# Performance work log

Hardware: AMD Instinct MI355X
Metric: run time of the kernel (lower is better)

The kernel has to match this reference:

```python
import jax, jax.numpy as jnp
import numpy as np

B, F, V, E, H, L, D = 1024, 4096, 20000, 512, 1024, 20, 4


def _lstm_step(x, h, c, Wih, Whh, bih, bhh):
    # torch nn.LSTMCell gate order: i, f, g, o
    gates = x @ Wih.T + bih + h @ Whh.T + bhh
    i, f, g, o = jnp.split(gates, 4, axis=-1)
    c = jax.nn.sigmoid(f) * c + jax.nn.sigmoid(i) * jnp.tanh(g)
    h = jax.nn.sigmoid(o) * jnp.tanh(c)
    return h, c


def setup_inputs() -> dict:
    key = jax.random.key(0)
    ks = jax.random.split(key, 12)
    s = 0.02  # small init so exp(scores) stays sane
    return {
        "target": jax.random.normal(ks[0], (B, F), jnp.float32),
        "distractors": jax.random.normal(ks[1], (D, B, F), jnp.float32),
        "start_token_idx": 1,
        "max_sentence_length": L,
        # Sender params
        "emb_s": jax.random.normal(ks[2], (V, E), jnp.float32) * s,
        "Wih_s": jax.random.normal(ks[3], (4 * H, E), jnp.float32) * s,
        "Whh_s": jax.random.normal(ks[4], (4 * H, H), jnp.float32) * s,
        "bih_s": jnp.zeros((4 * H,), jnp.float32),
        "bhh_s": jnp.zeros((4 * H,), jnp.float32),
        "aff_s_W": jax.random.normal(ks[5], (H, F), jnp.float32) * s,
        "aff_s_b": jnp.zeros((H,), jnp.float32),
        "probs_W": jax.random.normal(ks[6], (V, H), jnp.float32) * s,
        "probs_b": jnp.zeros((V,), jnp.float32),
        # Receiver params
        "emb_r": jax.random.normal(ks[7], (V, E), jnp.float32) * s,
        "Wih_r": jax.random.normal(ks[8], (4 * H, E), jnp.float32) * s,
        "Whh_r": jax.random.normal(ks[9], (4 * H, H), jnp.float32) * s,
        "bih_r": jnp.zeros((4 * H,), jnp.float32),
        "bhh_r": jnp.zeros((4 * H,), jnp.float32),
        "aff_r_W": jax.random.normal(ks[10], (F, H), jnp.float32) * s,
        "aff_r_b": jnp.zeros((F,), jnp.float32),
    }


def reference(target, distractors, start_token_idx, max_sentence_length,
              emb_s, Wih_s, Whh_s, bih_s, bhh_s, aff_s_W, aff_s_b, probs_W, probs_b,
              emb_r, Wih_r, Whh_r, bih_r, bhh_r, aff_r_W, aff_r_b):
    b = target.shape[0]
    # ---- Sender (greedy / eval path): per-step LSTMCell as lax.scan ----
    h0 = target @ aff_s_W.T + aff_s_b              # [B, H]
    c0 = jnp.zeros_like(h0)
    w0 = jnp.broadcast_to(emb_s[start_token_idx], (b, emb_s.shape[1]))

    def s_step(carry, _):
        h, c, w = carry
        h, c = _lstm_step(w, h, c, Wih_s, Whh_s, bih_s, bhh_s)
        logits = h @ probs_W.T + probs_b            # [B, V]
        logp = jax.nn.log_softmax(logits, axis=-1)
        w_idx = jnp.argmax(logits, axis=-1)         # greedy token
        lp = jnp.take_along_axis(logp, w_idx[:, None], axis=1)[:, 0]
        return (h, c, emb_s[w_idx]), (w_idx, lp)

    _, (message, lps) = jax.lax.scan(s_step, (h0, c0, w0), None, length=max_sentence_length)
    log_prob = lps[-1]                              # log_prob of last sampled token, [B]

    # ---- Receiver: consume message tokens with second LSTMCell scan ----
    def r_step(carry, w_idx):
        h, c = carry
        h, c = _lstm_step(emb_r[w_idx], h, c, Wih_r, Whh_r, bih_r, bhh_r)
        return (h, c), None

    (hr, _), _ = jax.lax.scan(r_step, (jnp.zeros_like(h0), jnp.zeros_like(h0)), message)
    r = hr @ aff_r_W.T + aff_r_b                    # [B, F]

    # ---- Hinge loss over distractors ----
    r_t = r.T                                       # [F, B]
    ts = target @ r_t                               # [B, B]
    ds = jnp.einsum('dbf,fk->dbk', distractors, r_t)  # [D, B, B]
    hinge = jnp.maximum(0.0, 1.0 - ts[None] + ds).sum(0)  # [B, B]
    loss = jnp.mean(jnp.mean(-hinge * log_prob[None, :], axis=1))

    target_prob = jnp.mean(jnp.exp(ts), axis=1)     # [B]
    dist_prob = jnp.mean(jnp.exp(ds), axis=2)       # [D, B]
    all_probs = jnp.concatenate([target_prob[:, None], dist_prob.T], axis=1)  # [B, 1+D]
    accuracy = jnp.mean((jnp.argmax(all_probs, axis=1) == 0).astype(jnp.float32))
    return loss, accuracy
```

## Files before the change

kernel.cpp:

```cpp
#include <hip/hip_runtime.h>
#include <cmath>

#define B_ 1024
#define F_ 4096
#define V_ 20000
#define E_ 512
#define H_ 1024
#define L_ 20
#define D_ 4

typedef __bf16 bf16x8 __attribute__((ext_vector_type(8)));
typedef float  f32x4  __attribute__((ext_vector_type(4)));

#define BM 128
#define BN 128
#define BK 32

#define VPAD 20096

__device__ __forceinline__ void remap_block(int& bm, int& bn)
{
    const int nbx  = gridDim.x;
    const int nby  = gridDim.y;
    const int nwg  = nbx * nby;
    const int flat = blockIdx.y * nbx + blockIdx.x;
    const int q = nwg >> 3, r = nwg & 7;
    const int xcd = flat & 7, lead = flat >> 3;
    const int wgid = (xcd < r ? xcd * (q + 1) : r * (q + 1) + (xcd - r) * q) + lead;
    bm = (wgid % nby) * BM;
    bn = (wgid / nby) * BN;
}

__device__ __forceinline__ void gld_lds16(const void* g, void* l)
{
    __builtin_amdgcn_global_load_lds(
        (const __attribute__((address_space(1))) void*)g,
        (__attribute__((address_space(3))) void*)l, 16, 0, 0);
}

__global__ __launch_bounds__(256, 2) void gemm_nt_split(
    const float* __restrict__ A1, const float* __restrict__ W1, int K1,
    const float* __restrict__ A2, const float* __restrict__ W2, int K2,
    const float* __restrict__ b1, const float* __restrict__ b2,
    float* __restrict__ C, int M, int N)
{
    __shared__ __align__(16) __bf16 As_hi[BM][BK];
    __shared__ __align__(16) __bf16 As_lo[BM][BK];
    __shared__ __align__(16) __bf16 Ws_hi[BN][BK];
    __shared__ __align__(16) __bf16 Ws_lo[BN][BK];

    const int tid  = threadIdx.x;
    int bm, bn;
    remap_block(bm, bn);
    const int srow = tid >> 1;
    const int scol = (tid & 1) * 16;
    const int lane = tid & 63;
    const int wv   = tid >> 6;
    const int wm   = (wv & 1) * 64;
    const int wn   = (wv >> 1) * 64;
    const int fm   = lane & 15;
    const int fq   = lane >> 4;

    const bool wok = (bn + srow) < N;

    f32x4 acc[4][4];
#pragma unroll
    for (int i = 0; i < 4; ++i)
#pragma unroll
        for (int j = 0; j < 4; ++j) acc[i][j] = (f32x4){0.f, 0.f, 0.f, 0.f};

#pragma unroll 1
    for (int s = 0; s < 2; ++s) {
        const float* A = s ? A2 : A1;
        const float* W = s ? W2 : W1;
        const int    K = s ? K2 : K1;
        if (!A) continue;
        const float* Arow = A + (size_t)(bm + srow) * K;
        const float* Wrow = W + (size_t)(bn + srow) * K;

        for (int k0 = 0; k0 < K; k0 += BK) {
            float av[16], wvv[16];
            const float* ap = Arow + k0 + scol;
            *(float4*)&av[0]   = *(const float4*)(ap + 0);
            *(float4*)&av[4]   = *(const float4*)(ap + 4);
            *(float4*)&av[8]   = *(const float4*)(ap + 8);
            *(float4*)&av[12]  = *(const float4*)(ap + 12);
            if (wok) {
                const float* wp = Wrow + k0 + scol;
                *(float4*)&wvv[0]  = *(const float4*)(wp + 0);
                *(float4*)&wvv[4]  = *(const float4*)(wp + 4);
                *(float4*)&wvv[8]  = *(const float4*)(wp + 8);
                *(float4*)&wvv[12] = *(const float4*)(wp + 12);
            } else {
#pragma unroll
                for (int v = 0; v < 16; ++v) wvv[v] = 0.f;
            }
            __syncthreads();

#pragma unroll
            for (int u = 0; u < 16; u += 8) {
                bf16x8 hh, ll;
#pragma unroll
                for (int v = 0; v < 8; ++v) {
                    float x = av[u + v];
                    __bf16 h = (__bf16)x;
                    hh[v] = h;
                    ll[v] = (__bf16)(x - (float)h);
                }
                *(bf16x8*)&As_hi[srow][scol + u] = hh;
                *(bf16x8*)&As_lo[srow][scol + u] = ll;
            }
#pragma unroll
            for (int u = 0; u < 16; u += 8) {
                bf16x8 hh, ll;
#pragma unroll
                for (int v = 0; v < 8; ++v) {
                    float x = wvv[u + v];
                    __bf16 h = (__bf16)x;
                    hh[v] = h;
                    ll[v] = (__bf16)(x - (float)h);
                }
                *(bf16x8*)&Ws_hi[srow][scol + u] = hh;
                *(bf16x8*)&Ws_lo[srow][scol + u] = ll;
            }
            __syncthreads();

            bf16x8 ah[4], al[4];
#pragma unroll
            for (int i = 0; i < 4; ++i) {
                ah[i] = *(const bf16x8*)&As_hi[wm + i * 16 + fm][fq * 8];
                al[i] = *(const bf16x8*)&As_lo[wm + i * 16 + fm][fq * 8];
            }
#pragma unroll
            for (int j = 0; j < 4; ++j) {
                bf16x8 bh = *(const bf16x8*)&Ws_hi[wn + j * 16 + fm][fq * 8];
                bf16x8 bl = *(const bf16x8*)&Ws_lo[wn + j * 16 + fm][fq * 8];
#pragma unroll
                for (int i = 0; i < 4; ++i) {
                    acc[i][j] = __builtin_amdgcn_mfma_f32_16x16x32_bf16(
                        al[i], bh, acc[i][j], 0, 0, 0);
                    acc[i][j] = __builtin_amdgcn_mfma_f32_16x16x32_bf16(
                        ah[i], bl, acc[i][j], 0, 0, 0);
                    acc[i][j] = __builtin_amdgcn_mfma_f32_16x16x32_bf16(
                        ah[i], bh, acc[i][j], 0, 0, 0);
                }
            }
        }
    }

#pragma unroll
    for (int j = 0; j < 4; ++j) {
        int col = bn + wn + j * 16 + fm;
        if (col >= N) continue;
        float badd = (b1 ? b1[col] : 0.f) + (b2 ? b2[col] : 0.f);
#pragma unroll
        for (int i = 0; i < 4; ++i) {
            int row0 = bm + wm + i * 16 + fq * 4;
            f32x4 v = acc[i][j];
#pragma unroll
            for (int r = 0; r < 4; ++r)
                C[(size_t)(row0 + r) * N + col] = v[r] + badd;
        }
    }
}

__global__ __launch_bounds__(256, 3) void gemm_nt_planes(
    const __bf16* __restrict__ Ah1, const __bf16* __restrict__ Al1,
    const __bf16* __restrict__ Wh1, const __bf16* __restrict__ Wl1, int K1,
    const __bf16* __restrict__ Ah2, const __bf16* __restrict__ Al2,
    const __bf16* __restrict__ Wh2, const __bf16* __restrict__ Wl2, int K2,
    const float* __restrict__ b1, const float* __restrict__ b2,
    float* __restrict__ C, int M, int N)
{
    __shared__ __align__(16) __bf16 As_hi[BM][BK];
    __shared__ __align__(16) __bf16 As_lo[BM][BK];
    __shared__ __align__(16) __bf16 Ws_hi[BN][BK];
    __shared__ __align__(16) __bf16 Ws_lo[BN][BK];

    const int tid  = threadIdx.x;
    int bm, bn;
    remap_block(bm, bn);
    const int srow = tid >> 2;
    const int scol = (tid & 3) * 8;
    const int lane = tid & 63;
    const int wv   = tid >> 6;
    const int wm   = (wv & 1) * 64;
    const int wn   = (wv >> 1) * 64;
    const int fm   = lane & 15;
    const int fq   = lane >> 4;

    f32x4 acc[4][4];
#pragma unroll
    for (int i = 0; i < 4; ++i)
#pragma unroll
        for (int j = 0; j < 4; ++j) acc[i][j] = (f32x4){0.f, 0.f, 0.f, 0.f};

#pragma unroll 1
    for (int s = 0; s < 2; ++s) {
        const __bf16* Ah = s ? Ah2 : Ah1;
        const __bf16* Al = s ? Al2 : Al1;
        const __bf16* Wh = s ? Wh2 : Wh1;
        const __bf16* Wl = s ? Wl2 : Wl1;
        const int     K  = s ? K2  : K1;
        if (!Ah) continue;
        const size_t aoff  = (size_t)(bm + srow) * K + scol;
        const size_t woff  = (size_t)(bn + srow) * K + scol;
        const size_t step  = (size_t)64 * K;

        for (int k0 = 0; k0 < K; k0 += BK) {
            __syncthreads();
            gld_lds16(Ah + aoff + k0,        &As_hi[srow][scol]);
            gld_lds16(Ah + aoff + k0 + step, &As_hi[srow + 64][scol]);
            gld_lds16(Al + aoff + k0,        &As_lo[srow][scol]);
            gld_lds16(Al + aoff + k0 + step, &As_lo[srow + 64][scol]);
            gld_lds16(Wh + woff + k0,        &Ws_hi[srow][scol]);
            gld_lds16(Wh + woff + k0 + step, &Ws_hi[srow + 64][scol]);
            gld_lds16(Wl + woff + k0,        &Ws_lo[srow][scol]);
            gld_lds16(Wl + woff + k0 + step, &Ws_lo[srow + 64][scol]);
            __syncthreads();

            bf16x8 ah[4], al[4];
#pragma unroll
            for (int i = 0; i < 4; ++i) {
                ah[i] = *(const bf16x8*)&As_hi[wm + i * 16 + fm][fq * 8];
                al[i] = *(const bf16x8*)&As_lo[wm + i * 16 + fm][fq * 8];
            }
#pragma unroll
            for (int j = 0; j < 4; ++j) {
                bf16x8 bh = *(const bf16x8*)&Ws_hi[wn + j * 16 + fm][fq * 8];
                bf16x8 bl = *(const bf16x8*)&Ws_lo[wn + j * 16 + fm][fq * 8];
#pragma unroll
                for (int i = 0; i < 4; ++i) {
                    acc[i][j] = __builtin_amdgcn_mfma_f32_16x16x32_bf16(
                        al[i], bh, acc[i][j], 0, 0, 0);
                    acc[i][j] = __builtin_amdgcn_mfma_f32_16x16x32_bf16(
                        ah[i], bl, acc[i][j], 0, 0, 0);
                    acc[i][j] = __builtin_amdgcn_mfma_f32_16x16x32_bf16(
                        ah[i], bh, acc[i][j], 0, 0, 0);
                }
            }
        }
    }

#pragma unroll
    for (int j = 0; j < 4; ++j) {
        int col = bn + wn + j * 16 + fm;
        if (col >= N) continue;
        float badd = (b1 ? b1[col] : 0.f) + (b2 ? b2[col] : 0.f);
#pragma unroll
        for (int i = 0; i < 4; ++i) {
            int row0 = bm + wm + i * 16 + fq * 4;
            f32x4 v = acc[i][j];
#pragma unroll
            for (int r = 0; r < 4; ++r)
                C[(size_t)(row0 + r) * N + col] = v[r] + badd;
        }
    }
}

__global__ __launch_bounds__(256) void split_planes(
    const float* __restrict__ src, __bf16* __restrict__ hi,
    __bf16* __restrict__ lo, long n8)
{
    long i = (long)blockIdx.x * 256 + threadIdx.x;
    if (i >= n8) return;
    float4 a = ((const float4*)src)[2 * i];
    float4 b = ((const float4*)src)[2 * i + 1];
    float v[8] = {a.x, a.y, a.z, a.w, b.x, b.y, b.z, b.w};
    bf16x8 hh, ll;
#pragma unroll
    for (int j = 0; j < 8; ++j) {
        float x = v[j];
        __bf16 h = (__bf16)x;
        hh[j] = h;
        ll[j] = (__bf16)(x - (float)h);
    }
    ((bf16x8*)hi)[i] = hh;
    ((bf16x8*)lo)[i] = ll;
}

__global__ __launch_bounds__(256) void lstm_pointwise(
    const float* __restrict__ gates, float* __restrict__ c, float* __restrict__ h,
    __bf16* __restrict__ hhi, __bf16* __restrict__ hlo)
{
    int i = blockIdx.x * blockDim.x + threadIdx.x;
    if (i >= B_ * H_) return;
    int b = i / H_, k = i % H_;
    const float* g = gates + (size_t)b * 4 * H_;
    float gi = g[k], gf = g[H_ + k], gg = g[2 * H_ + k], go = g[3 * H_ + k];
    float si = 1.f / (1.f + expf(-gi));
    float sf = 1.f / (1.f + expf(-gf));
    float so = 1.f / (1.f + expf(-go));
    float cn = sf * c[i] + si * tanhf(gg);
    c[i] = cn;
    float hv = so * tanhf(cn);
    h[i] = hv;
    if (hhi) {
        __bf16 hh = (__bf16)hv;
        hhi[i] = hh;
        hlo[i] = (__bf16)(hv - (float)hh);
    }
}

__global__ __launch_bounds__(256) void row_argmax_lse(
    const float* __restrict__ logits, int* __restrict__ tok,
    float* __restrict__ lp, int need_lp)
{
    int b = blockIdx.x;
    const float4* row4 = (const float4*)(logits + (size_t)b * V_);
    int tid = threadIdx.x;
    float m = -INFINITY; int mi = 0;
    float lm = -INFINITY, ls = 0.f;
    for (int j4 = tid; j4 < V_ / 4; j4 += 256) {
        float4 q = row4[j4];
        float vv[4] = {q.x, q.y, q.z, q.w};
#pragma unroll
        for (int u = 0; u < 4; ++u) {
            float v = vv[u];
            if (v > m) { m = v; mi = j4 * 4 + u; }
            if (need_lp) {
                if (v > lm) { ls = ls * expf(lm - v) + 1.f; lm = v; }
                else ls += expf(v - lm);
            }
        }
    }
    __shared__ float sm[256]; __shared__ int si[256];
    __shared__ float slm[256], sls[256];
    sm[tid] = m; si[tid] = mi; slm[tid] = lm; sls[tid] = ls;
    __syncthreads();
    for (int s = 128; s > 0; s >>= 1) {
        if (tid < s) {
            float vm = sm[tid + s]; int vi = si[tid + s];
            if (vm > sm[tid] || (vm == sm[tid] && vi < si[tid])) {
                sm[tid] = vm; si[tid] = vi;
            }
            if (need_lp) {
                float am = slm[tid], as = sls[tid];
                float bm2 = slm[tid + s], bs = sls[tid + s];
                if (am >= bm2) {
                    sls[tid] = as + bs * expf(bm2 - am);
                } else {
                    sls[tid] = bs + as * expf(am - bm2);
                    slm[tid] = bm2;
                }
            }
        }
        __syncthreads();
    }
    if (tid == 0) {
        tok[b] = si[0];
        if (need_lp) lp[b] = sm[0] - (slm[0] + logf(sls[0]));
    }
}

__global__ __launch_bounds__(128) void gather_emb(
    const float* __restrict__ emb, const int* __restrict__ tok,
    float* __restrict__ out)
{
    int b = blockIdx.x;
    int t = tok[b];
    const float4* src = (const float4*)(emb + (size_t)t * E_);
    float4* dst = (float4*)(out + (size_t)b * E_);
    for (int e = threadIdx.x; e < E_ / 4; e += blockDim.x) dst[e] = src[e];
}

__global__ __launch_bounds__(128) void broadcast_emb(
    const float* __restrict__ emb, const int* __restrict__ sidx,
    float* __restrict__ out)
{
    int b = blockIdx.x;
    int t = sidx[0];
    const float4* src = (const float4*)(emb + (size_t)t * E_);
    float4* dst = (float4*)(out + (size_t)b * E_);
    for (int e = threadIdx.x; e < E_ / 4; e += blockDim.x) dst[e] = src[e];
}

__device__ __forceinline__ void emb_row_split(
    const float* __restrict__ emb, int t, int b, int i,
    __bf16* __restrict__ whi, __bf16* __restrict__ wlo)
{
    const float4* src = (const float4*)(emb + (size_t)t * E_);
    float4 a = src[2 * i], c2 = src[2 * i + 1];
    float v[8] = {a.x, a.y, a.z, a.w, c2.x, c2.y, c2.z, c2.w};
    bf16x8 hh, ll;
#pragma unroll
    for (int j = 0; j < 8; ++j) {
        float x = v[j];
        __bf16 h = (__bf16)x;
        hh[j] = h;
        ll[j] = (__bf16)(x - (float)h);
    }
    ((bf16x8*)(whi + (size_t)b * E_))[i] = hh;
    ((bf16x8*)(wlo + (size_t)b * E_))[i] = ll;
}

__global__ __launch_bounds__(64) void gather_emb_planes(
    const float* __restrict__ emb, const int* __restrict__ tok,
    __bf16* __restrict__ whi, __bf16* __restrict__ wlo)
{
    emb_row_split(emb, tok[blockIdx.x], blockIdx.x, threadIdx.x, whi, wlo);
}

__global__ __launch_bounds__(64) void broadcast_emb_planes(
    const float* __restrict__ emb, const int* __restrict__ sidx,
    __bf16* __restrict__ whi, __bf16* __restrict__ wlo)
{
    emb_row_split(emb, sidx[0], blockIdx.x, threadIdx.x, whi, wlo);
}

__global__ __launch_bounds__(256) void zero_f32(float* __restrict__ p, int n)
{
    int i = blockIdx.x * blockDim.x + threadIdx.x;
    if (i < n) p[i] = 0.f;
}

__global__ __launch_bounds__(256) void loss_rows(
    const float* __restrict__ sc, const float* __restrict__ lp,
    float* __restrict__ loss_part, float* __restrict__ acc_flag)
{
    int i = blockIdx.x; int tid = threadIdx.x;
    const float* tsrow = sc + (size_t)i * B_;
    float lsum = 0.f, tps = 0.f;
    float dps[4] = {0.f, 0.f, 0.f, 0.f};
    for (int j = tid; j < B_; j += 256) {
        float tsv = tsrow[j];
        float hv = 0.f;
#pragma unroll
        for (int d = 0; d < 4; ++d) {
            float dv = sc[((size_t)(1 + d) * B_ + i) * B_ + j];
            float t = 1.f - tsv + dv;
            hv += (t > 0.f) ? t : 0.f;
            dps[d] += expf(dv);
        }
        lsum += hv * lp[j];
        tps += expf(tsv);
    }
    __shared__ float red[6][256];
    red[0][tid] = lsum; red[1][tid] = tps;
    red[2][tid] = dps[0]; red[3][tid] = dps[1];
    red[4][tid] = dps[2]; red[5][tid] = dps[3];
    __syncthreads();
    for (int s = 128; s > 0; s >>= 1) {
        if (tid < s) {
#pragma unroll
            for (int q = 0; q < 6; ++q) red[q][tid] += red[q][tid + s];
        }
        __syncthreads();
    }
    if (tid == 0) {
        loss_part[i] = -red[0][0];
        float tp = red[1][0];
        float mx = fmaxf(fmaxf(red[2][0], red[3][0]), fmaxf(red[4][0], red[5][0]));
        acc_flag[i] = (tp >= mx) ? 1.f : 0.f;
    }
}

__global__ __launch_bounds__(256) void finalize_k(
    const float* __restrict__ loss_part, const float* __restrict__ acc_flag,
    float* __restrict__ out)
{
    int tid = threadIdx.x;
    float ls = 0.f, ac = 0.f;
    for (int i = tid; i < B_; i += 256) { ls += loss_part[i]; ac += acc_flag[i]; }
    __shared__ float s1[256], s2[256];
    s1[tid] = ls; s2[tid] = ac;
    __syncthreads();
    for (int s = 128; s > 0; s >>= 1) {
        if (tid < s) { s1[tid] += s1[tid + s]; s2[tid] += s2[tid + s]; }
        __syncthreads();
    }
    if (tid == 0) {
        out[0] = s1[0] / ((float)B_ * (float)B_);
        out[1] = s2[0] / (float)B_;
    }
}

extern "C" void kernel_launch(void* const* d_in, const int* in_sizes, int n_in,
                              void* d_out, int out_size, void* d_ws, size_t ws_size,
                              hipStream_t stream)
{
    const float* target    = (const float*)d_in[0];
    const float* distract  = (const float*)d_in[1];
    const int*   start_tok = (const int*)d_in[2];
    const float* emb_s   = (const float*)d_in[4];
    const float* Wih_s   = (const float*)d_in[5];
    const float* Whh_s   = (const float*)d_in[6];
    const float* bih_s   = (const float*)d_in[7];
    const float* bhh_s   = (const float*)d_in[8];
    const float* aff_s_W = (const float*)d_in[9];
    const float* aff_s_b = (const float*)d_in[10];
    const float* probs_W = (const float*)d_in[11];
    const float* probs_b = (const float*)d_in[12];
    const float* emb_r   = (const float*)d_in[13];
    const float* Wih_r   = (const float*)d_in[14];
    const float* Whh_r   = (const float*)d_in[15];
    const float* bih_r   = (const float*)d_in[16];
    const float* bhh_r   = (const float*)d_in[17];
    const float* aff_r_W = (const float*)d_in[18];
    const float* aff_r_b = (const float*)d_in[19];

    float* ws = (float*)d_ws;
    const size_t OFF_HS     = 0;
    const size_t OFF_CS     = 1048576;
    const size_t OFF_WE     = 2097152;
    const size_t OFF_GATES  = 2621440;
    const size_t OFF_HR     = 6815744;
    const size_t OFF_CR     = 7864320;
    const size_t OFF_LP     = 8912896;
    const size_t OFF_LOSSP  = 8916992;
    const size_t OFF_ACCF   = 8921088;
    const size_t OFF_MSG    = 8925184;
    const size_t OFF_LOGITS = 9437184;
    const size_t OFF_R      = 9437184;
    const size_t OFF_SC     = 13631488;
    const size_t OFF_PROBS_HI = 29917184;
    const size_t OFF_PROBS_LO = 40206336;
    const size_t OFF_WIHS_HI  = 50495488;
    const size_t OFF_WIHS_LO  = 51544064;
    const size_t OFF_WHHS_HI  = 52592640;
    const size_t OFF_WHHS_LO  = 54689792;
    const size_t OFF_WIHR_HI  = 56786944;
    const size_t OFF_WIHR_LO  = 57835520;
    const size_t OFF_WHHR_HI  = 58884096;
    const size_t OFF_WHHR_LO  = 60981248;
    const size_t OFF_WEP_HI   = 63078400;
    const size_t OFF_WEP_LO   = 63340544;
    const size_t OFF_HSP_HI   = 63602688;
    const size_t OFF_HSP_LO   = 64126976;
    const size_t OFF_HRP_HI   = 64651264;
    const size_t OFF_HRP_LO   = 65175552;
    const size_t TOTAL_FLOATS = 65699840;

    float* h_s    = ws + OFF_HS;
    float* c_s    = ws + OFF_CS;
    float* w_e    = ws + OFF_WE;
    float* gates  = ws + OFF_GATES;
    float* h_r    = ws + OFF_HR;
    float* c_r    = ws + OFF_CR;
    float* lp     = ws + OFF_LP;
    float* lossp  = ws + OFF_LOSSP;
    float* accf   = ws + OFF_ACCF;
    int*   msg    = (int*)(ws + OFF_MSG);
    float* logits = ws + OFF_LOGITS;
    float* r_buf  = ws + OFF_R;
    float* sc     = ws + OFF_SC;

    auto gemm = [&](const float* A1, const float* W1, int K1,
                    const float* A2, const float* W2, int K2,
                    const float* b1, const float* b2,
                    float* C, int M, int N) {
        dim3 grid((N + BN - 1) / BN, M / BM);
        gemm_nt_split<<<grid, dim3(256), 0, stream>>>(A1, W1, K1, A2, W2, K2,
                                                      b1, b2, C, M, N);
    };

    const bool fast = ws_size >= TOTAL_FLOATS * sizeof(float);

    if (fast) {
        __bf16* probs_hi = (__bf16*)(ws + OFF_PROBS_HI);
        __bf16* probs_lo = (__bf16*)(ws + OFF_PROBS_LO);
        __bf16* wihs_hi  = (__bf16*)(ws + OFF_WIHS_HI);
        __bf16* wihs_lo  = (__bf16*)(ws + OFF_WIHS_LO);
        __bf16* whhs_hi  = (__bf16*)(ws + OFF_WHHS_HI);
        __bf16* whhs_lo  = (__bf16*)(ws + OFF_WHHS_LO);
        __bf16* wihr_hi  = (__bf16*)(ws + OFF_WIHR_HI);
        __bf16* wihr_lo  = (__bf16*)(ws + OFF_WIHR_LO);
        __bf16* whhr_hi  = (__bf16*)(ws + OFF_WHHR_HI);
        __bf16* whhr_lo  = (__bf16*)(ws + OFF_WHHR_LO);
        __bf16* we_hi    = (__bf16*)(ws + OFF_WEP_HI);
        __bf16* we_lo    = (__bf16*)(ws + OFF_WEP_LO);
        __bf16* hs_hi    = (__bf16*)(ws + OFF_HSP_HI);
        __bf16* hs_lo    = (__bf16*)(ws + OFF_HSP_LO);
        __bf16* hr_hi    = (__bf16*)(ws + OFF_HRP_HI);
        __bf16* hr_lo    = (__bf16*)(ws + OFF_HRP_LO);

        auto cvt = [&](const float* src, __bf16* hi, __bf16* lo, long n) {
            long n8 = n / 8;
            split_planes<<<(unsigned)((n8 + 255) / 256), 256, 0, stream>>>(
                src, hi, lo, n8);
        };
        auto gemmP = [&](const __bf16* Ah1, const __bf16* Al1,
                         const __bf16* Wh1, const __bf16* Wl1, int K1,
                         const __bf16* Ah2, const __bf16* Al2,
                         const __bf16* Wh2, const __bf16* Wl2, int K2,
                         const float* b1, const float* b2,
                         float* C, int M, int N) {
            dim3 grid((N + BN - 1) / BN, M / BM);
            gemm_nt_planes<<<grid, dim3(256), 0, stream>>>(
                Ah1, Al1, Wh1, Wl1, K1, Ah2, Al2, Wh2, Wl2, K2, b1, b2, C, M, N);
        };

        cvt(probs_W, probs_hi, probs_lo, (long)V_ * H_);
        cvt(Wih_s, wihs_hi, wihs_lo, (long)4 * H_ * E_);
        cvt(Whh_s, whhs_hi, whhs_lo, (long)4 * H_ * H_);
        cvt(Wih_r, wihr_hi, wihr_lo, (long)4 * H_ * E_);
        cvt(Whh_r, whhr_hi, whhr_lo, (long)4 * H_ * H_);
        {
            int padn = (VPAD - V_) * H_ / 2;
            zero_f32<<<(padn + 255) / 256, 256, 0, stream>>>(
                ws + OFF_PROBS_HI + (size_t)V_ * H_ / 2, padn);
            zero_f32<<<(padn + 255) / 256, 256, 0, stream>>>(
                ws + OFF_PROBS_LO + (size_t)V_ * H_ / 2, padn);
        }

        gemm(target, aff_s_W, F_, nullptr, nullptr, 0, aff_s_b, nullptr, h_s, B_, H_);
        cvt(h_s, hs_hi, hs_lo, (long)B_ * H_);
        zero_f32<<<(B_ * H_ + 255) / 256, 256, 0, stream>>>(c_s, B_ * H_);
        broadcast_emb_planes<<<B_, 64, 0, stream>>>(emb_s, start_tok, we_hi, we_lo);

        for (int t = 0; t < L_; ++t) {
            gemmP(we_hi, we_lo, wihs_hi, wihs_lo, E_,
                  hs_hi, hs_lo, whhs_hi, whhs_lo, H_,
                  bih_s, bhh_s, gates, B_, 4 * H_);
            lstm_pointwise<<<(B_ * H_ + 255) / 256, 256, 0, stream>>>(
                gates, c_s, h_s, hs_hi, hs_lo);
            gemmP(hs_hi, hs_lo, probs_hi, probs_lo, H_,
                  nullptr, nullptr, nullptr, nullptr, 0,
                  probs_b, nullptr, logits, B_, V_);
            row_argmax_lse<<<B_, 256, 0, stream>>>(logits, msg + (size_t)t * B_, lp,
                                                   (t == L_ - 1) ? 1 : 0);
            if (t < L_ - 1)
                gather_emb_planes<<<B_, 64, 0, stream>>>(emb_s, msg + (size_t)t * B_,
                                                         we_hi, we_lo);
        }

        zero_f32<<<(B_ * H_ + 255) / 256, 256, 0, stream>>>(h_r, B_ * H_);
        zero_f32<<<(B_ * H_ + 255) / 256, 256, 0, stream>>>(c_r, B_ * H_);
        zero_f32<<<(B_ * H_ / 2 + 255) / 256, 256, 0, stream>>>(
            ws + OFF_HRP_HI, B_ * H_ / 2);
        zero_f32<<<(B_ * H_ / 2 + 255) / 256, 256, 0, stream>>>(
            ws + OFF_HRP_LO, B_ * H_ / 2);
        for (int t = 0; t < L_; ++t) {
            gather_emb_planes<<<B_, 64, 0, stream>>>(emb_r, msg + (size_t)t * B_,
                                                     we_hi, we_lo);
            gemmP(we_hi, we_lo, wihr_hi, wihr_lo, E_,
                  hr_hi, hr_lo, whhr_hi, whhr_lo, H_,
                  bih_r, bhh_r, gates, B_, 4 * H_);
            lstm_pointwise<<<(B_ * H_ + 255) / 256, 256, 0, stream>>>(
                gates, c_r, h_r, hr_hi, hr_lo);
        }
    } else {
        gemm(target, aff_s_W, F_, nullptr, nullptr, 0, aff_s_b, nullptr, h_s, B_, H_);
        zero_f32<<<(B_ * H_ + 255) / 256, 256, 0, stream>>>(c_s, B_ * H_);
        broadcast_emb<<<B_, 128, 0, stream>>>(emb_s, start_tok, w_e);

        for (int t = 0; t < L_; ++t) {
            gemm(w_e, Wih_s, E_, h_s, Whh_s, H_, bih_s, bhh_s, gates, B_, 4 * H_);
            lstm_pointwise<<<(B_ * H_ + 255) / 256, 256, 0, stream>>>(
                gates, c_s, h_s, nullptr, nullptr);
            gemm(h_s, probs_W, H_, nullptr, nullptr, 0, probs_b, nullptr,
                 logits, B_, V_);
            row_argmax_lse<<<B_, 256, 0, stream>>>(logits, msg + (size_t)t * B_, lp,
                                                   (t == L_ - 1) ? 1 : 0);
            if (t < L_ - 1)
                gather_emb<<<B_, 128, 0, stream>>>(emb_s, msg + (size_t)t * B_, w_e);
        }

        zero_f32<<<(B_ * H_ + 255) / 256, 256, 0, stream>>>(h_r, B_ * H_);
        zero_f32<<<(B_ * H_ + 255) / 256, 256, 0, stream>>>(c_r, B_ * H_);
        for (int t = 0; t < L_; ++t) {
            gather_emb<<<B_, 128, 0, stream>>>(emb_r, msg + (size_t)t * B_, w_e);
            gemm(w_e, Wih_r, E_, h_r, Whh_r, H_, bih_r, bhh_r, gates, B_, 4 * H_);
            lstm_pointwise<<<(B_ * H_ + 255) / 256, 256, 0, stream>>>(
                gates, c_r, h_r, nullptr, nullptr);
        }
    }

    gemm(h_r, aff_r_W, H_, nullptr, nullptr, 0, aff_r_b, nullptr, r_buf, B_, F_);
    gemm(target, r_buf, F_, nullptr, nullptr, 0, nullptr, nullptr, sc, B_, B_);
    gemm(distract, r_buf, F_, nullptr, nullptr, 0, nullptr, nullptr,
         sc + (size_t)B_ * B_, D_ * B_, B_);

    loss_rows<<<B_, 256, 0, stream>>>(sc, lp, lossp, accf);
    finalize_k<<<1, 256, 0, stream>>>(lossp, accf, (float*)d_out);
}
```

Measured before the change: 6.718 ms.

## Use pre-split bf16 planes for tail GEMMs and 128x64 tiles for gate GEMMs

Templates the plane-based GEMM on tile shape and adds a 128x64 variant. The LSTM gate GEMMs (N=4096) switch to it to get more workgroups. When the workspace is large enough, the affine, receiver-output and score GEMMs are moved from the on-the-fly fp32 split kernel to precomputed hi/lo bf16 planes, and the target and distractor score GEMMs are merged into one launch. The split GEMM loses its XCD remap. The cost is extra conversion passes over target, distractors and the affine weights, plus a larger workspace requirement.

Result: faster. 6.216 ms (-7.5%).

```diff
diff --git a/kernel.cpp b/kernel.cpp
--- a/kernel.cpp
+++ b/kernel.cpp
@@ -18,19 +18,6 @@
 
 #define VPAD 20096
 
-__device__ __forceinline__ void remap_block(int& bm, int& bn)
-{
-    const int nbx  = gridDim.x;
-    const int nby  = gridDim.y;
-    const int nwg  = nbx * nby;
-    const int flat = blockIdx.y * nbx + blockIdx.x;
-    const int q = nwg >> 3, r = nwg & 7;
-    const int xcd = flat & 7, lead = flat >> 3;
-    const int wgid = (xcd < r ? xcd * (q + 1) : r * (q + 1) + (xcd - r) * q) + lead;
-    bm = (wgid % nby) * BM;
-    bn = (wgid / nby) * BN;
-}
-
 __device__ __forceinline__ void gld_lds16(const void* g, void* l)
 {
     __builtin_amdgcn_global_load_lds(
@@ -50,8 +37,8 @@
     __shared__ __align__(16) __bf16 Ws_lo[BN][BK];
 
     const int tid  = threadIdx.x;
-    int bm, bn;
-    remap_block(bm, bn);
+    const int bm   = blockIdx.y * BM;
+    const int bn   = blockIdx.x * BN;
     const int srow = tid >> 1;
     const int scol = (tid & 1) * 16;
     const int lane = tid & 63;
@@ -164,7 +151,8 @@
     }
 }
 
-__global__ __launch_bounds__(256, 3) void gemm_nt_planes(
+template<int TBM, int TBN>
+__global__ __launch_bounds__(256, 3) void gemm_nt_planes_t(
     const __bf16* __restrict__ Ah1, const __bf16* __restrict__ Al1,
     const __bf16* __restrict__ Wh1, const __bf16* __restrict__ Wl1, int K1,
     const __bf16* __restrict__ Ah2, const __bf16* __restrict__ Al2,
@@ -172,28 +160,39 @@
     const float* __restrict__ b1, const float* __restrict__ b2,
     float* __restrict__ C, int M, int N)
 {
-    __shared__ __align__(16) __bf16 As_hi[BM][BK];
-    __shared__ __align__(16) __bf16 As_lo[BM][BK];
-    __shared__ __align__(16) __bf16 Ws_hi[BN][BK];
-    __shared__ __align__(16) __bf16 Ws_lo[BN][BK];
+    constexpr int MI = TBM / 32;
+    constexpr int NJ = TBN / 32;
+
+    __shared__ __align__(16) __bf16 As_hi[TBM][BK];
+    __shared__ __align__(16) __bf16 As_lo[TBM][BK];
+    __shared__ __align__(16) __bf16 Ws_hi[TBN][BK];
+    __shared__ __align__(16) __bf16 Ws_lo[TBN][BK];
 
     const int tid  = threadIdx.x;
-    int bm, bn;
-    remap_block(bm, bn);
+    const int nbx  = gridDim.x;
+    const int nby  = gridDim.y;
+    const int nwg  = nbx * nby;
+    const int flat = blockIdx.y * nbx + blockIdx.x;
+    const int q = nwg >> 3, r = nwg & 7;
+    const int xcd = flat & 7, lead = flat >> 3;
+    const int wgid = (xcd < r ? xcd * (q + 1) : r * (q + 1) + (xcd - r) * q) + lead;
+    const int bm = (wgid % nby) * TBM;
+    const int bn = (wgid / nby) * TBN;
+
     const int srow = tid >> 2;
     const int scol = (tid & 3) * 8;
     const int lane = tid & 63;
     const int wv   = tid >> 6;
-    const int wm   = (wv & 1) * 64;
-    const int wn   = (wv >> 1) * 64;
+    const int wm   = (wv & 1) * (TBM / 2);
+    const int wn   = (wv >> 1) * (TBN / 2);
     const int fm   = lane & 15;
     const int fq   = lane >> 4;
 
-    f32x4 acc[4][4];
-#pragma unroll
-    for (int i = 0; i < 4; ++i)
-#pragma unroll
-        for (int j = 0; j < 4; ++j) acc[i][j] = (f32x4){0.f, 0.f, 0.f, 0.f};
+    f32x4 acc[MI][NJ];
+#pragma unroll
+    for (int i = 0; i < MI; ++i)
+#pragma unroll
+        for (int j = 0; j < NJ; ++j) acc[i][j] = (f32x4){0.f, 0.f, 0.f, 0.f};
 
 #pragma unroll 1
     for (int s = 0; s < 2; ++s) {
@@ -203,34 +202,35 @@
         const __bf16* Wl = s ? Wl2 : Wl1;
         const int     K  = s ? K2  : K1;
         if (!Ah) continue;
-        const size_t aoff  = (size_t)(bm + srow) * K + scol;
-        const size_t woff  = (size_t)(bn + srow) * K + scol;
-        const size_t step  = (size_t)64 * K;
+        const size_t aoff = (size_t)(bm + srow) * K + scol;
+        const size_t woff = (size_t)(bn + srow) * K + scol;
 
         for (int k0 = 0; k0 < K; k0 += BK) {
             __syncthreads();
-            gld_lds16(Ah + aoff + k0,        &As_hi[srow][scol]);
-            gld_lds16(Ah + aoff + k0 + step, &As_hi[srow + 64][scol]);
-            gld_lds16(Al + aoff + k0,        &As_lo[srow][scol]);
-            gld_lds16(Al + aoff + k0 + step, &As_lo[srow + 64][scol]);
-            gld_lds16(Wh + woff + k0,        &Ws_hi[srow][scol]);
-            gld_lds16(Wh + woff + k0 + step, &Ws_hi[srow + 64][scol]);
-            gld_lds16(Wl + woff + k0,        &Ws_lo[srow][scol]);
-            gld_lds16(Wl + woff + k0 + step, &Ws_lo[srow + 64][scol]);
+#pragma unroll
+            for (int u = 0; u < TBM; u += 64) {
+                gld_lds16(Ah + aoff + k0 + (size_t)u * K, &As_hi[srow + u][scol]);
+                gld_lds16(Al + aoff + k0 + (size_t)u * K, &As_lo[srow + u][scol]);
+            }
+#pragma unroll
+            for (int u = 0; u < TBN; u += 64) {
+                gld_lds16(Wh + woff + k0 + (size_t)u * K, &Ws_hi[srow + u][scol]);
+                gld_lds16(Wl + woff + k0 + (size_t)u * K, &Ws_lo[srow + u][scol]);
+            }
             __syncthreads();
 
-            bf16x8 ah[4], al[4];
-#pragma unroll
-            for (int i = 0; i < 4; ++i) {
+            bf16x8 ah[MI], al[MI];
+#pragma unroll
+            for (int i = 0; i < MI; ++i) {
                 ah[i] = *(const bf16x8*)&As_hi[wm + i * 16 + fm][fq * 8];
                 al[i] = *(const bf16x8*)&As_lo[wm + i * 16 + fm][fq * 8];
             }
 #pragma unroll
-            for (int j = 0; j < 4; ++j) {
+            for (int j = 0; j < NJ; ++j) {
                 bf16x8 bh = *(const bf16x8*)&Ws_hi[wn + j * 16 + fm][fq * 8];
                 bf16x8 bl = *(const bf16x8*)&Ws_lo[wn + j * 16 + fm][fq * 8];
 #pragma unroll
-                for (int i = 0; i < 4; ++i) {
+                for (int i = 0; i < MI; ++i) {
                     acc[i][j] = __builtin_amdgcn_mfma_f32_16x16x32_bf16(
                         al[i], bh, acc[i][j], 0, 0, 0);
                     acc[i][j] = __builtin_amdgcn_mfma_f32_16x16x32_bf16(
@@ -243,17 +243,17 @@
     }
 
 #pragma unroll
-    for (int j = 0; j < 4; ++j) {
+    for (int j = 0; j < NJ; ++j) {
         int col = bn + wn + j * 16 + fm;
         if (col >= N) continue;
         float badd = (b1 ? b1[col] : 0.f) + (b2 ? b2[col] : 0.f);
 #pragma unroll
-        for (int i = 0; i < 4; ++i) {
+        for (int i = 0; i < MI; ++i) {
             int row0 = bm + wm + i * 16 + fq * 4;
             f32x4 v = acc[i][j];
 #pragma unroll
-            for (int r = 0; r < 4; ++r)
-                C[(size_t)(row0 + r) * N + col] = v[r] + badd;
+            for (int rr = 0; rr < 4; ++rr)
+                C[(size_t)(row0 + rr) * N + col] = v[rr] + badd;
         }
     }
 }
@@ -530,6 +530,15 @@
     const size_t OFF_HRP_HI   = 64651264;
     const size_t OFF_HRP_LO   = 65175552;
     const size_t TOTAL_FLOATS = 65699840;
+    const size_t OFF_AFFS_HI = 65699840;
+    const size_t OFF_AFFS_LO = 67796992;
+    const size_t OFF_AFFR_HI = 69894144;
+    const size_t OFF_AFFR_LO = 71991296;
+    const size_t OFF_RP_HI   = 74088448;
+    const size_t OFF_RP_LO   = 76185600;
+    const size_t OFF_TD_HI   = 78282752;
+    const size_t OFF_TD_LO   = 88768512;
+    const size_t TOTAL2_FLOATS = 99254272;
 
     float* h_s    = ws + OFF_HS;
     float* c_s    = ws + OFF_CS;
@@ -554,7 +563,8 @@
                                                       b1, b2, C, M, N);
     };
 
-    const bool fast = ws_size >= TOTAL_FLOATS * sizeof(float);
+    const bool fast      = ws_size >= TOTAL_FLOATS * sizeof(float);
+    const bool fast_tail = ws_size >= TOTAL2_FLOATS * sizeof(float);
 
     if (fast) {
         __bf16* probs_hi = (__bf16*)(ws + OFF_PROBS_HI);
@@ -573,6 +583,14 @@
         __bf16* hs_lo    = (__bf16*)(ws + OFF_HSP_LO);
         __bf16* hr_hi    = (__bf16*)(ws + OFF_HRP_HI);
         __bf16* hr_lo    = (__bf16*)(ws + OFF_HRP_LO);
+        __bf16* affs_hi  = (__bf16*)(ws + OFF_AFFS_HI);
+        __bf16* affs_lo  = (__bf16*)(ws + OFF_AFFS_LO);
+        __bf16* affr_hi  = (__bf16*)(ws + OFF_AFFR_HI);
+        __bf16* affr_lo  = (__bf16*)(ws + OFF_AFFR_LO);
+        __bf16* rp_hi    = (__bf16*)(ws + OFF_RP_HI);
+        __bf16* rp_lo    = (__bf16*)(ws + OFF_RP_LO);
+        __bf16* td_hi    = (__bf16*)(ws + OFF_TD_HI);
+        __bf16* td_lo    = (__bf16*)(ws + OFF_TD_LO);
 
         auto cvt = [&](const float* src, __bf16* hi, __bf16* lo, long n) {
             long n8 = n / 8;
@@ -586,7 +604,17 @@
                          const float* b1, const float* b2,
                          float* C, int M, int N) {
             dim3 grid((N + BN - 1) / BN, M / BM);
-            gemm_nt_planes<<<grid, dim3(256), 0, stream>>>(
+            gemm_nt_planes_t<128, 128><<<grid, dim3(256), 0, stream>>>(
+                Ah1, Al1, Wh1, Wl1, K1, Ah2, Al2, Wh2, Wl2, K2, b1, b2, C, M, N);
+        };
+        auto gemmP64 = [&](const __bf16* Ah1, const __bf16* Al1,
+                           const __bf16* Wh1, const __bf16* Wl1, int K1,
+                           const __bf16* Ah2, const __bf16* Al2,
+                           const __bf16* Wh2, const __bf16* Wl2, int K2,
+                           const float* b1, const float* b2,
+                           float* C, int M, int N) {
+            dim3 grid((N + 63) / 64, M / BM);
+            gemm_nt_planes_t<128, 64><<<grid, dim3(256), 0, stream>>>(
                 Ah1, Al1, Wh1, Wl1, K1, Ah2, Al2, Wh2, Wl2, K2, b1, b2, C, M, N);
         };
 
@@ -602,16 +630,29 @@
             zero_f32<<<(padn + 255) / 256, 256, 0, stream>>>(
                 ws + OFF_PROBS_LO + (size_t)V_ * H_ / 2, padn);
         }
-
-        gemm(target, aff_s_W, F_, nullptr, nullptr, 0, aff_s_b, nullptr, h_s, B_, H_);
+        if (fast_tail) {
+            cvt(aff_s_W, affs_hi, affs_lo, (long)H_ * F_);
+            cvt(aff_r_W, affr_hi, affr_lo, (long)F_ * H_);
+            cvt(target, td_hi, td_lo, (long)B_ * F_);
+            cvt(distract, td_hi + (size_t)B_ * F_, td_lo + (size_t)B_ * F_,
+                (long)D_ * B_ * F_);
+        }
+
+        if (fast_tail)
+            gemmP64(td_hi, td_lo, affs_hi, affs_lo, F_,
+                    nullptr, nullptr, nullptr, nullptr, 0,
+                    aff_s_b, nullptr, h_s, B_, H_);
+        else
+            gemm(target, aff_s_W, F_, nullptr, nullptr, 0, aff_s_b, nullptr,
+                 h_s, B_, H_);
         cvt(h_s, hs_hi, hs_lo, (long)B_ * H_);
         zero_f32<<<(B_ * H_ + 255) / 256, 256, 0, stream>>>(c_s, B_ * H_);
         broadcast_emb_planes<<<B_, 64, 0, stream>>>(emb_s, start_tok, we_hi, we_lo);
 
         for (int t = 0; t < L_; ++t) {
-            gemmP(we_hi, we_lo, wihs_hi, wihs_lo, E_,
-                  hs_hi, hs_lo, whhs_hi, whhs_lo, H_,
-                  bih_s, bhh_s, gates, B_, 4 * H_);
+            gemmP64(we_hi, we_lo, wihs_hi, wihs_lo, E_,
+                    hs_hi, hs_lo, whhs_hi, whhs_lo, H_,
+                    bih_s, bhh_s, gates, B_, 4 * H_);
             lstm_pointwise<<<(B_ * H_ + 255) / 256, 256, 0, stream>>>(
                 gates, c_s, h_s, hs_hi, hs_lo);
             gemmP(hs_hi, hs_lo, probs_hi, probs_lo, H_,
@@ -633,11 +674,28 @@
         for (int t = 0; t < L_; ++t) {
             gather_emb_planes<<<B_, 64, 0, stream>>>(emb_r, msg + (size_t)t * B_,
                                                      we_hi, we_lo);
-            gemmP(we_hi, we_lo, wihr_hi, wihr_lo, E_,
-                  hr_hi, hr_lo, whhr_hi, whhr_lo, H_,
-                  bih_r, bhh_r, gates, B_, 4 * H_);
+            gemmP64(we_hi, we_lo, wihr_hi, wihr_lo, E_,
+                    hr_hi, hr_lo, whhr_hi, whhr_lo, H_,
+                    bih_r, bhh_r, gates, B_, 4 * H_);
             lstm_pointwise<<<(B_ * H_ + 255) / 256, 256, 0, stream>>>(
                 gates, c_r, h_r, hr_hi, hr_lo);
+        }
+
+        if (fast_tail) {
+            gemmP64(hr_hi, hr_lo, affr_hi, affr_lo, H_,
+                    nullptr, nullptr, nullptr, nullptr, 0,
+                    aff_r_b, nullptr, r_buf, B_, F_);
+            cvt(r_buf, rp_hi, rp_lo, (long)B_ * F_);
+            gemmP64(td_hi, td_lo, rp_hi, rp_lo, F_,
+                    nullptr, nullptr, nullptr, nullptr, 0,
+                    nullptr, nullptr, sc, (1 + D_) * B_, B_);
+        } else {
+            gemm(h_r, aff_r_W, H_, nullptr, nullptr, 0, aff_r_b, nullptr,
+                 r_buf, B_, F_);
+            gemm(target, r_buf, F_, nullptr, nullptr, 0, nullptr, nullptr,
+                 sc, B_, B_);
+            gemm(distract, r_buf, F_, nullptr, nullptr, 0, nullptr, nullptr,
+                 sc + (size_t)B_ * B_, D_ * B_, B_);
         }
     } else {
         gemm(target, aff_s_W, F_, nullptr, nullptr, 0, aff_s_b, nullptr, h_s, B_, H_);
@@ -664,12 +722,12 @@
             lstm_pointwise<<<(B_ * H_ + 255) / 256, 256, 0, stream>>>(
                 gates, c_r, h_r, nullptr, nullptr);
         }
-    }
-
-    gemm(h_r, aff_r_W, H_, nullptr, nullptr, 0, aff_r_b, nullptr, r_buf, B_, F_);
-    gemm(target, r_buf, F_, nullptr, nullptr, 0, nullptr, nullptr, sc, B_, B_);
-    gemm(distract, r_buf, F_, nullptr, nullptr, 0, nullptr, nullptr,
-         sc + (size_t)B_ * B_, D_ * B_, B_);
+
+        gemm(h_r, aff_r_W, H_, nullptr, nullptr, 0, aff_r_b, nullptr, r_buf, B_, F_);
+        gemm(target, r_buf, F_, nullptr, nullptr, 0, nullptr, nullptr, sc, B_, B_);
+        gemm(distract, r_buf, F_, nullptr, nullptr, 0, nullptr, nullptr,
+             sc + (size_t)B_ * B_, D_ * B_, B_);
+    }
 
     loss_rows<<<B_, 256, 0, stream>>>(sc, lp, lossp, accf);
     finalize_k<<<1, 256, 0, stream>>>(lossp, accf, (float*)d_out);
```
